# Kernel tuning notes

Hardware: AMD Instinct MI355X
Metric: run time of the kernel (lower is better)

The kernel has to match this reference:

```python
import jax, jax.numpy as jnp
import numpy as np

MARGIN = 0.25
GAMMA = 256.0
NEG_INF = -1e30


def setup_inputs() -> dict:
    key = jax.random.key(0)
    k1, k2 = jax.random.split(key)
    B, D = 8192, 128
    return {
        "embeddings_a": jax.random.normal(k1, (B, D), dtype=jnp.float32),
        "embeddings_b": jax.random.normal(k2, (B, D), dtype=jnp.float32),
    }


def _l2_normalize(x, eps=1e-12):
    # matches F.normalize(p=2, dim=1): x / max(||x||, eps)
    n = jnp.sqrt(jnp.sum(x * x, axis=1, keepdims=True))
    return x / jnp.maximum(n, eps)


def reference(embeddings_a, embeddings_b):
    B = embeddings_a.shape[0]
    a = _l2_normalize(embeddings_a)
    b = _l2_normalize(embeddings_b)
    sim = a @ b.T  # [B, B]

    pos_mask = jnp.eye(B, dtype=bool)  # labels=None path

    # positive logits: -gamma * relu((1-m) - s) * (s - m)
    logit_pos = -GAMMA * jnp.maximum((1.0 - MARGIN) - sim, 0.0) * (sim - MARGIN)
    # negative logits:  gamma * relu(s - m) * (s + m)
    logit_neg = GAMMA * jnp.maximum(sim - MARGIN, 0.0) * (sim + MARGIN)

    # masked per-row logsumexp over positive / negative sets
    lse_pos = jax.nn.logsumexp(jnp.where(pos_mask, logit_pos, NEG_INF), axis=1)
    lse_neg = jax.nn.logsumexp(jnp.where(pos_mask, NEG_INF, logit_neg), axis=1)

    losses = jax.nn.softplus(lse_pos + lse_neg)  # [B]
    return jnp.mean(losses)  # reduction='mean'
```

## Files before the change

kernel.cpp:

```cpp
#include <hip/hip_runtime.h>


#define B_N 8192
#define D_K 128
#define MARGIN 0.25f
#define M2 (MARGIN * MARGIN)
#define GAMMA 256.0f

#define BM 128
#define BN 64
#define NCH 16
#define CPB (B_N / NCH)
#define NSUB (CPB / BN)
#define NROWBLK 32

typedef __attribute__((ext_vector_type(8))) short short8;
typedef __attribute__((ext_vector_type(4))) float f32x4;

__device__ __forceinline__ unsigned short f2bf(float x) {
  unsigned u = __float_as_uint(x);
  u += 0x7FFFu + ((u >> 16) & 1u);
  return (unsigned short)(u >> 16);
}

__device__ __forceinline__ void gload_lds16(const void* gsrc, void* ldst) {
  __builtin_amdgcn_global_load_lds(
      (const __attribute__((address_space(1))) void*)gsrc,
      (__attribute__((address_space(3))) void*)ldst, 16, 0, 0);
}

__global__ __launch_bounds__(256) void norm_diag_kernel(
    const float* __restrict__ a, const float* __restrict__ b,
    unsigned short* __restrict__ abf, unsigned short* __restrict__ bbf,
    float* __restrict__ diag) {
  int wave = threadIdx.x >> 6, lane = threadIdx.x & 63;
  int r = blockIdx.x * 4 + wave;
  int half = lane >> 5, l32 = lane & 31;
  const float* src = half ? b : a;
  unsigned short* dst = half ? bbf : abf;

  float4 v = ((const float4*)(src + (size_t)r * D_K))[l32];
  float ss = v.x * v.x + v.y * v.y + v.z * v.z + v.w * v.w;
  #pragma unroll
  for (int m = 16; m >= 1; m >>= 1) ss += __shfl_xor(ss, m);
  float inv = 1.0f / fmaxf(sqrtf(ss), 1e-12f);
  float n0 = v.x * inv, n1 = v.y * inv, n2 = v.z * inv, n3 = v.w * inv;

  ushort4 o = {f2bf(n0), f2bf(n1), f2bf(n2), f2bf(n3)};
  ((ushort4*)(dst + (size_t)r * D_K))[l32] = o;

  float d = n0 * __shfl_xor(n0, 32) + n1 * __shfl_xor(n1, 32) +
            n2 * __shfl_xor(n2, 32) + n3 * __shfl_xor(n3, 32);
  #pragma unroll
  for (int m = 16; m >= 1; m >>= 1) d += __shfl_xor(d, m);
  if (lane == 0) diag[r] = d;
}

__global__ __launch_bounds__(256, 4) void simlse_kernel(
    const unsigned short* __restrict__ abf, const unsigned short* __restrict__ bbf,
    float* __restrict__ partS) {
  __shared__ __align__(16) unsigned short L[2][BN * D_K];

  const int tid = threadIdx.x;
  const int wave = tid >> 6, lane = tid & 63;
  const int r16 = lane & 15, kq = lane >> 4;
  const int rowBase = blockIdx.y * BM;
  const int chunk = blockIdx.x;

  int stageOff[4];
  #pragma unroll
  for (int it = 0; it < 4; ++it) {
    int g = it * 256 + tid;
    int row = g >> 4, sl = g & 15;
    stageOff[it] = row * D_K + (sl ^ (row & 7)) * 8;
  }

  #pragma unroll
  for (int half = 0; half < 2; ++half) {
    const unsigned short* srcA = abf + (size_t)(rowBase + half * 64) * D_K;
    #pragma unroll
    for (int it = 0; it < 4; ++it)
      gload_lds16(srcA + stageOff[it], &L[half][(it * 256 + wave * 64) * 8]);
  }
  __syncthreads();

  short8 af[2][4];
  #pragma unroll
  for (int mi = 0; mi < 2; ++mi) {
    int row = wave * 32 + mi * 16 + r16;
    const unsigned short* Abuf = L[row >> 6];
    int lrow = row & 63;
    #pragma unroll
    for (int ks = 0; ks < 4; ++ks) {
      int slot = (ks * 4 + kq) ^ (lrow & 7);
      af[mi][ks] = *(const short8*)&Abuf[lrow * D_K + slot * 8];
    }
  }
  __syncthreads();

  #pragma unroll
  for (int h = 0; h < 2; ++h) {
    const unsigned short* srcB = bbf + (size_t)(chunk * CPB + h * BN) * D_K;
    #pragma unroll
    for (int it = 0; it < 4; ++it)
      gload_lds16(srcB + stageOff[it], &L[h][(it * 256 + wave * 64) * 8]);
  }
  __syncthreads();

  float Ssum[2][4];
  #pragma unroll
  for (int mi = 0; mi < 2; ++mi)
    #pragma unroll
    for (int r = 0; r < 4; ++r) Ssum[mi][r] = 0.0f;

  #pragma unroll 2
  for (int st = 0; st < NSUB; ++st) {
    const unsigned short* cb = L[st & 1];

    f32x4 acc[2][4];
    const f32x4 z4 = {0.f, 0.f, 0.f, 0.f};
    #pragma unroll
    for (int mi = 0; mi < 2; ++mi)
      #pragma unroll
      for (int ni = 0; ni < 4; ++ni) acc[mi][ni] = z4;

    #pragma unroll
    for (int ks = 0; ks < 4; ++ks) {
      short8 bf[4];
      #pragma unroll
      for (int ni = 0; ni < 4; ++ni) {
        int row = ni * 16 + r16;
        int slot = (ks * 4 + kq) ^ (row & 7);
        bf[ni] = *(const short8*)&cb[row * D_K + slot * 8];
      }
      #pragma unroll
      for (int mi = 0; mi < 2; ++mi)
        #pragma unroll
        for (int ni = 0; ni < 4; ++ni)
          acc[mi][ni] = __builtin_amdgcn_mfma_f32_16x16x32_bf16(
              af[mi][ks], bf[ni], acc[mi][ni], 0, 0, 0);
    }

    #pragma unroll
    for (int mi = 0; mi < 2; ++mi)
      #pragma unroll
      for (int ni = 0; ni < 4; ++ni) {
        f32x4 v = acc[mi][ni];
        float mx = fmaxf(fmaxf(v[0], v[1]), fmaxf(v[2], v[3]));
        if (__any(mx > MARGIN)) {
          #pragma unroll
          for (int r = 0; r < 4; ++r) {
            float s = v[r];
            float t = fmaf(s, s, -M2);
            float z = (s > MARGIN) ? GAMMA * t : 0.0f;
            Ssum[mi][r] += __expf(z) - 1.0f;
          }
        }
      }

    __syncthreads();

    if (st + 2 < NSUB) {
      const unsigned short* srcB =
          bbf + (size_t)(chunk * CPB + (st + 2) * BN) * D_K;
      unsigned short* dstB = (unsigned short*)L[st & 1];
      #pragma unroll
      for (int it = 0; it < 4; ++it)
        gload_lds16(srcB + stageOff[it], &dstB[(it * 256 + wave * 64) * 8]);
    }
  }

  #pragma unroll
  for (int mi = 0; mi < 2; ++mi)
    #pragma unroll
    for (int r = 0; r < 4; ++r) {
      float v = Ssum[mi][r];
      v += __shfl_xor(v, 1);
      v += __shfl_xor(v, 2);
      v += __shfl_xor(v, 4);
      v += __shfl_xor(v, 8);
      if (r16 == 0)
        partS[(size_t)chunk * B_N + rowBase + wave * 32 + mi * 16 + kq * 4 + r] = v;
    }
}

__global__ __launch_bounds__(256) void rowfin_kernel(
    const float* __restrict__ partS, const float* __restrict__ diag,
    float* __restrict__ bpart) {
  __shared__ float red[4];
  int tid = threadIdx.x, lane = tid & 63, wid = tid >> 6;
  int i = blockIdx.x * 256 + tid;
  float S = 0.0f;
  #pragma unroll
  for (int c = 0; c < NCH; ++c) S += partS[(size_t)c * B_N + i];
  float sd = diag[i];
  float zd = (sd > MARGIN) ? GAMMA * fmaf(sd, sd, -M2) : 0.0f;
  float ed = __expf(zd);
  float lneg = __logf((float)B_N + S - ed);
  float lpos = -GAMMA * fmaxf((1.0f - MARGIN) - sd, 0.0f) * (sd - MARGIN);
  float x = lpos + lneg;
  float acc = fmaxf(x, 0.0f) + log1pf(__expf(-fabsf(x)));
  #pragma unroll
  for (int m = 32; m >= 1; m >>= 1) acc += __shfl_xor(acc, m);
  if (lane == 0) red[wid] = acc;
  __syncthreads();
  if (tid == 0) bpart[blockIdx.x] = red[0] + red[1] + red[2] + red[3];
}

__global__ __launch_bounds__(64) void mean_kernel(
    const float* __restrict__ bpart, float* __restrict__ out) {
  int lane = threadIdx.x;
  float v = (lane < 32) ? bpart[lane] : 0.0f;
  #pragma unroll
  for (int m = 32; m >= 1; m >>= 1) v += __shfl_xor(v, m);
  if (lane == 0) out[0] = v * (1.0f / B_N);
}

extern "C" void kernel_launch(void* const* d_in, const int* in_sizes, int n_in,
                              void* d_out, int out_size, void* d_ws, size_t ws_size,
                              hipStream_t stream) {
  const float* a = (const float*)d_in[0];
  const float* b = (const float*)d_in[1];
  float* out = (float*)d_out;

  char* w = (char*)d_ws;
  unsigned short* abf = (unsigned short*)w;
  unsigned short* bbf = (unsigned short*)(w + (size_t)B_N * D_K * 2);
  float* partS = (float*)(w + (size_t)B_N * D_K * 4);
  float* diag = partS + (size_t)NCH * B_N;
  float* bpart = diag + B_N;

  norm_diag_kernel<<<B_N / 4, 256, 0, stream>>>(a, b, abf, bbf, diag);
  simlse_kernel<<<dim3(NCH, B_N / BM), 256, 0, stream>>>(abf, bbf, partS);
  rowfin_kernel<<<NROWBLK, 256, 0, stream>>>(partS, diag, bpart);
  mean_kernel<<<1, 64, 0, stream>>>(bpart, out);
}
```

Measured before the change: 37.17 us.

## Drop LDS staging, load MFMA operands from global, and remap blocks per XCD

The sim-LSE kernel stops staging A and B tiles through shared memory with global_load_lds and barriers. Each lane now reads its MFMA fragments straight from global memory, relying on L2/L1 caching. The launch becomes a 1D grid, with block IDs remapped so that each XCD handles two B chunks, to improve L2 locality of the B operand. This removes the LDS traffic and the per-stage syncs, but drops the double-buffered prefetch and exposes global load latency inside the MFMA loop.

Result: slower. 78.30 us (+110.7%).

```diff
diff --git a/kernel.cpp b/kernel.cpp
--- a/kernel.cpp
+++ b/kernel.cpp
@@ -21,12 +21,6 @@
   unsigned u = __float_as_uint(x);
   u += 0x7FFFu + ((u >> 16) & 1u);
   return (unsigned short)(u >> 16);
-}
-
-__device__ __forceinline__ void gload_lds16(const void* gsrc, void* ldst) {
-  __builtin_amdgcn_global_load_lds(
-      (const __attribute__((address_space(1))) void*)gsrc,
-      (__attribute__((address_space(3))) void*)ldst, 16, 0, 0);
 }
 
 __global__ __launch_bounds__(256) void norm_diag_kernel(
@@ -59,53 +53,29 @@
 __global__ __launch_bounds__(256, 4) void simlse_kernel(
     const unsigned short* __restrict__ abf, const unsigned short* __restrict__ bbf,
     float* __restrict__ partS) {
-  __shared__ __align__(16) unsigned short L[2][BN * D_K];
-
   const int tid = threadIdx.x;
   const int wave = tid >> 6, lane = tid & 63;
   const int r16 = lane & 15, kq = lane >> 4;
-  const int rowBase = blockIdx.y * BM;
-  const int chunk = blockIdx.x;
 
-  int stageOff[4];
-  #pragma unroll
-  for (int it = 0; it < 4; ++it) {
-    int g = it * 256 + tid;
-    int row = g >> 4, sl = g & 15;
-    stageOff[it] = row * D_K + (sl ^ (row & 7)) * 8;
-  }
-
-  #pragma unroll
-  for (int half = 0; half < 2; ++half) {
-    const unsigned short* srcA = abf + (size_t)(rowBase + half * 64) * D_K;
-    #pragma unroll
-    for (int it = 0; it < 4; ++it)
-      gload_lds16(srcA + stageOff[it], &L[half][(it * 256 + wave * 64) * 8]);
-  }
-  __syncthreads();
+  const int bid = blockIdx.x;
+  const int xcd = bid & 7, lid = bid >> 3;
+  const int chunk = xcd * 2 + (lid >> 6);
+  const int rowBase = (lid & 63) * BM;
 
   short8 af[2][4];
   #pragma unroll
   for (int mi = 0; mi < 2; ++mi) {
-    int row = wave * 32 + mi * 16 + r16;
-    const unsigned short* Abuf = L[row >> 6];
-    int lrow = row & 63;
+    const unsigned short* arow =
+        abf + (size_t)(rowBase + wave * 32 + mi * 16 + r16) * D_K;
     #pragma unroll
-    for (int ks = 0; ks < 4; ++ks) {
-      int slot = (ks * 4 + kq) ^ (lrow & 7);
-      af[mi][ks] = *(const short8*)&Abuf[lrow * D_K + slot * 8];
-    }
+    for (int ks = 0; ks < 4; ++ks)
+      af[mi][ks] = *(const short8*)&arow[(ks * 4 + kq) * 8];
   }
-  __syncthreads();
 
+  const unsigned short* bptr[4];
   #pragma unroll
-  for (int h = 0; h < 2; ++h) {
-    const unsigned short* srcB = bbf + (size_t)(chunk * CPB + h * BN) * D_K;
-    #pragma unroll
-    for (int it = 0; it < 4; ++it)
-      gload_lds16(srcB + stageOff[it], &L[h][(it * 256 + wave * 64) * 8]);
-  }
-  __syncthreads();
+  for (int ni = 0; ni < 4; ++ni)
+    bptr[ni] = bbf + (size_t)(chunk * CPB + ni * 16 + r16) * D_K + kq * 8;
 
   float Ssum[2][4];
   #pragma unroll
@@ -115,8 +85,6 @@
 
   #pragma unroll 2
   for (int st = 0; st < NSUB; ++st) {
-    const unsigned short* cb = L[st & 1];
-
     f32x4 acc[2][4];
     const f32x4 z4 = {0.f, 0.f, 0.f, 0.f};
     #pragma unroll
@@ -128,11 +96,8 @@
     for (int ks = 0; ks < 4; ++ks) {
       short8 bf[4];
       #pragma unroll
-      for (int ni = 0; ni < 4; ++ni) {
-        int row = ni * 16 + r16;
-        int slot = (ks * 4 + kq) ^ (row & 7);
-        bf[ni] = *(const short8*)&cb[row * D_K + slot * 8];
-      }
+      for (int ni = 0; ni < 4; ++ni)
+        bf[ni] = *(const short8*)(bptr[ni] + ks * 32);
       #pragma unroll
       for (int mi = 0; mi < 2; ++mi)
         #pragma unroll
@@ -158,16 +123,8 @@
         }
       }
 
-    __syncthreads();
-
-    if (st + 2 < NSUB) {
-      const unsigned short* srcB =
-          bbf + (size_t)(chunk * CPB + (st + 2) * BN) * D_K;
-      unsigned short* dstB = (unsigned short*)L[st & 1];
-      #pragma unroll
-      for (int it = 0; it < 4; ++it)
-        gload_lds16(srcB + stageOff[it], &dstB[(it * 256 + wave * 64) * 8]);
-    }
+    #pragma unroll
+    for (int ni = 0; ni < 4; ++ni) bptr[ni] += BN * D_K;
   }
 
   #pragma unroll
@@ -231,7 +188,7 @@
   float* bpart = diag + B_N;
 
   norm_diag_kernel<<<B_N / 4, 256, 0, stream>>>(a, b, abf, bbf, diag);
-  simlse_kernel<<<dim3(NCH, B_N / BM), 256, 0, stream>>>(abf, bbf, partS);
+  simlse_kernel<<<NCH * (B_N / BM), 256, 0, stream>>>(abf, bbf, partS);
   rowfin_kernel<<<NROWBLK, 256, 0, stream>>>(partS, diag, bpart);
   mean_kernel<<<1, 64, 0, stream>>>(bpart, out);
 }
```
